# Optimization experiments

Measured on AMD Instinct MI355X. Metric: run time of the kernel, lower is better.

The kernel has to match this reference:

```python
import jax, jax.numpy as jnp
import numpy as np

B, S, D_MODEL, N_HEAD = 8, 512, 1024, 16
HEAD_DIM = D_MODEL // N_HEAD


def _pos_embed(seq_len, dim):
    # RelativeSinusoidalPositionalEmbedding(dim, padding_idx=0, init_size=1200)
    num = 1201  # init_size + 1
    half = dim // 2
    freq = np.exp(np.arange(half, dtype=np.float32) * (-np.log(10000.0) / (half - 1)))
    pos = np.arange(-((num + 1) // 2), num // 2, dtype=np.float32)  # tf.range(-num//2, num//2), python floor div
    emb = pos[:, None] * freq[None, :]
    table = np.concatenate([np.sin(emb), np.cos(emb)], axis=1).astype(np.float32)  # [num, dim]
    table[0] = 0.0  # padding_idx = 0
    origin_shift = num // 2 + 1  # 601
    idx = np.arange(-seq_len, seq_len) + origin_shift
    return jnp.asarray(table[idx])  # [2*seq_len, dim]


def setup_inputs() -> dict:
    key = jax.random.key(0)
    k1, k2, k3, k4 = jax.random.split(key, 4)
    return {
        "x": jax.random.normal(k1, (B, S, D_MODEL), dtype=jnp.float32),
        "mask": jnp.ones((B, S), dtype=jnp.int32),
        "Wqv": jax.random.normal(k2, (D_MODEL, 2 * D_MODEL), dtype=jnp.float32) * 0.02,
        "r_r_bias": jax.random.normal(k3, (N_HEAD, HEAD_DIM), dtype=jnp.float32) * 0.02,
        "r_w_bias": jax.random.normal(k4, (N_HEAD, HEAD_DIM), dtype=jnp.float32) * 0.02,
    }


def _shift(BD):
    # [b, h, s, 2s] -> [b, h, s, s] via pad-reshape trick
    b, h, s, _ = BD.shape
    zp = jnp.zeros((b, h, s, 1), BD.dtype)
    BD = jnp.concatenate([BD, zp], axis=-1).reshape(b, h, 2 * s + 1, s)
    BD = BD[:, :, :-1].reshape(b, h, s, 2 * s)
    return BD[:, :, :, s:]


def reference(x, mask, Wqv, r_r_bias, r_w_bias):
    pos = _pos_embed(S, HEAD_DIM)  # [2S, head_dim], stop-gradient constant
    qv = x @ Wqv  # [B, S, 2*D]
    q, v = jnp.split(qv, 2, axis=-1)

    def heads(t):
        return t.reshape(B, S, N_HEAD, HEAD_DIM).transpose(0, 2, 1, 3)  # bhsd

    q, k, v = heads(q), heads(x), heads(v)
    rw_q = q + r_r_bias[None, :, None, :]
    AC = jnp.einsum('bhqd,bhkd->bhqk', rw_q, k)
    D_ = jnp.einsum('hd,ld->hl', r_w_bias, pos)[None, :, None, :]  # [1, h, 1, 2S]
    B_ = jnp.einsum('bhqd,ld->bhql', q, pos)  # [b, h, S, 2S]
    BD = _shift(B_ + D_)
    attn = AC + BD  # scale=False -> divide by 1
    m = mask.astype(jnp.float32)[:, None, None, :]
    attn = attn * m - (1.0 - m) * 1e8
    attn = jax.nn.softmax(attn, axis=-1)  # dropout is identity at inference
    out = jnp.einsum('bhqk,bhkd->bhqd', attn, v)
    return out.transpose(0, 2, 1, 3).reshape(B, S, D_MODEL)
```

## Files before the change

kernel.cpp:

```cpp
#include <hip/hip_runtime.h>


using h4 = __attribute__((ext_vector_type(4))) _Float16;
using h8 = __attribute__((ext_vector_type(8))) _Float16;
using f32x4 = __attribute__((ext_vector_type(4))) float;

#define MFMA16(a, b, c) __builtin_amdgcn_mfma_f32_16x16x32_f16((a), (b), (c), 0, 0, 0)

#define GLOAD_LDS16(gp, lp)                                                        \
  __builtin_amdgcn_global_load_lds(                                                \
      (const __attribute__((address_space(1))) unsigned int*)(gp),                 \
      (__attribute__((address_space(3))) unsigned int*)(lp), 16, 0, 0)

__global__ __launch_bounds__(256) void k_cast_x(const float* __restrict__ x,
                                                _Float16* __restrict__ xh) {
  size_t idx = (size_t)blockIdx.x * 256 + threadIdx.x;
  const float* src = x + idx * 8;
  _Float16 tmp[8];
#pragma unroll
  for (int j = 0; j < 8; ++j) tmp[j] = (_Float16)src[j];
  *(h8*)(xh + idx * 8) = *(const h8*)tmp;
}

__global__ __launch_bounds__(256) void k_posP(_Float16* __restrict__ posP) {
  int idx = blockIdx.x * 256 + threadIdx.x;
  int t = idx >> 6, j = idx & 63;
  int jj = j & 31;
  float f = expf((float)jj * (-9.210340371976184f / 31.0f));
  float ang = (float)t * f;
  posP[idx] = (_Float16)((j < 32) ? sinf(ang) : cosf(ang));
}

__global__ __launch_bounds__(256) void k_trans_w(const float* __restrict__ Wqv,
                                                 _Float16* __restrict__ wT) {
  __shared__ _Float16 t[64][72];
  int bk = blockIdx.x & 15, bn = blockIdx.x >> 4;
  int k0 = bk * 64, n0 = bn * 64;
  int r = threadIdx.x >> 2, c = (threadIdx.x & 3) * 16;
  const float* src = Wqv + (size_t)(k0 + r) * 2048 + n0 + c;
#pragma unroll
  for (int j = 0; j < 16; ++j) t[r][c + j] = (_Float16)src[j];
  __syncthreads();
  _Float16 tmp[16];
#pragma unroll
  for (int j = 0; j < 16; ++j) tmp[j] = t[c + j][r];
  _Float16* dst = wT + (size_t)(n0 + r) * 1024 + k0 + c;
  *(h8*)dst = *(const h8*)tmp;
  *(h8*)(dst + 8) = *(const h8*)(tmp + 8);
}

__global__ __launch_bounds__(256) void k_gemm(const _Float16* __restrict__ xh,
                                              const _Float16* __restrict__ wT,
                                              const float* __restrict__ rr,
                                              const float* __restrict__ rw,
                                              _Float16* __restrict__ qrr,
                                              _Float16* __restrict__ qrwp,
                                              _Float16* __restrict__ vT) {
  __shared__ _Float16 At[128 * 32];
  __shared__ _Float16 Bt[128 * 32];

  int bid = blockIdx.x;
  int bm = bid & 31, bn = bid >> 5;
  int tid = threadIdx.x;
  int w = tid >> 6, lane = tid & 63;
  int lr = lane & 15, lg = lane >> 4;

  const _Float16* gA = xh + (size_t)(bm * 128 + 32 * w + (lane >> 2)) * 1024 + (lane & 3) * 8;
  const _Float16* gB = wT + (size_t)(bn * 128 + 32 * w + (lane >> 2)) * 1024 + (lane & 3) * 8;
  _Float16* lA0 = &At[(32 * w) * 32];
  _Float16* lA1 = &At[(32 * w + 16) * 32];
  _Float16* lB0 = &Bt[(32 * w) * 32];
  _Float16* lB1 = &Bt[(32 * w + 16) * 32];

  int wm = w >> 1, wn = w & 1;
  const _Float16* la = &At[(wm * 64 + lr) * 32 + lg * 8];
  const _Float16* lb = &Bt[(wn * 64 + lr) * 32 + lg * 8];

  f32x4 acc[4][4] = {};

  for (int k0 = 0; k0 < 1024; k0 += 32) {
    GLOAD_LDS16(gA + k0, lA0);
    GLOAD_LDS16(gA + 16 * 1024 + k0, lA1);
    GLOAD_LDS16(gB + k0, lB0);
    GLOAD_LDS16(gB + 16 * 1024 + k0, lB1);
    __syncthreads();
    h8 af[4], bf[4];
#pragma unroll
    for (int mi = 0; mi < 4; ++mi) af[mi] = *(const h8*)(la + mi * 512);
#pragma unroll
    for (int ni = 0; ni < 4; ++ni) bf[ni] = *(const h8*)(lb + ni * 512);
#pragma unroll
    for (int mi = 0; mi < 4; ++mi)
#pragma unroll
      for (int ni = 0; ni < 4; ++ni)
        acc[mi][ni] = MFMA16(af[mi], bf[ni], acc[mi][ni]);
    __syncthreads();
  }

  int hg = bn * 2 + wn;
  int mb = bm * 128 + wm * 64;
  if (hg < 16) {
    int h = hg;
    float rrv[4], rwv[4];
#pragma unroll
    for (int ni = 0; ni < 4; ++ni) {
      rrv[ni] = rr[h * 64 + ni * 16 + lr];
      rwv[ni] = rw[h * 64 + ni * 16 + lr];
    }
    float f0 = expf((float)lr * (-9.210340371976184f / 31.0f));
    float f1 = expf((float)(16 + lr) * (-9.210340371976184f / 31.0f));
#pragma unroll
    for (int mi = 0; mi < 4; ++mi)
#pragma unroll
      for (int r = 0; r < 4; ++r) {
        int m = mb + mi * 16 + lg * 4 + r;
        int b = m >> 9, s = m & 511;
        size_t base = ((size_t)(b * 16 + h) * 512 + s) * 64;
#pragma unroll
        for (int ni = 0; ni < 4; ++ni)
          qrr[base + ni * 16 + lr] = (_Float16)(acc[mi][ni][r] + rrv[ni]);
        {
          float qs = acc[mi][0][r] + rwv[0], qc = acc[mi][2][r] + rwv[2];
          float sn, cs;
          sincosf((float)s * f0, &sn, &cs);
          qrwp[base + lr] = (_Float16)(qs * cs + qc * sn);
          qrwp[base + lr + 32] = (_Float16)(qc * cs - qs * sn);
        }
        {
          float qs = acc[mi][1][r] + rwv[1], qc = acc[mi][3][r] + rwv[3];
          float sn, cs;
          sincosf((float)s * f1, &sn, &cs);
          qrwp[base + 16 + lr] = (_Float16)(qs * cs + qc * sn);
          qrwp[base + 16 + lr + 32] = (_Float16)(qc * cs - qs * sn);
        }
      }
  } else {
    int h = hg - 16;
#pragma unroll
    for (int mi = 0; mi < 4; ++mi) {
      int m = mb + mi * 16 + lg * 4;
      int b = m >> 9, s0 = m & 511;
      size_t vtbase = (size_t)(b * 16 + h) * 64 * 512;
#pragma unroll
      for (int ni = 0; ni < 4; ++ni) {
        int d = ni * 16 + lr;
        _Float16 t4[4];
#pragma unroll
        for (int r = 0; r < 4; ++r) t4[r] = (_Float16)acc[mi][ni][r];
        *(h4*)(vT + vtbase + (size_t)d * 512 + s0) = *(const h4*)t4;
      }
    }
  }
}

__global__ __launch_bounds__(256, 2) void k_attn(const _Float16* __restrict__ xh,
                                                 const _Float16* __restrict__ qrr,
                                                 const _Float16* __restrict__ qrwp,
                                                 const _Float16* __restrict__ vT,
                                                 const _Float16* __restrict__ posPg,
                                                 const int* __restrict__ mask,
                                                 float* __restrict__ out) {
  __shared__ _Float16 Kp[128 * 128];
  __shared__ _Float16 Vt[64 * 128];
  __shared__ _Float16 Pl[4][16 * 136];
  __shared__ float Ms[512];

  int bid = blockIdx.x;
  int qb = bid >> 7, h = bid & 15, b = (bid >> 4) & 7;
  int q0 = qb * 64;
  int tid = threadIdx.x;
  int w = tid >> 6, lane = tid & 63;
  int lr = lane & 15, lg = lane >> 4;

  const size_t bh = (size_t)(b * 16 + h);
  const _Float16* qrr_p = qrr + (bh * 512 + q0 + 16 * w + lr) * 64 + lg * 8;
  const _Float16* qrw_p = qrwp + (bh * 512 + q0 + 16 * w + lr) * 64 + lg * 8;
  const _Float16* kb = xh + (size_t)b * 512 * 1024 + h * 64;
  const _Float16* vTp = vT + bh * 64 * 512;
  const int* mrow = mask + b * 512;

  Ms[tid] = (float)mrow[tid];
  Ms[tid + 256] = (float)mrow[tid + 256];

  h8 ar0 = *(const h8*)(qrr_p);
  h8 ar1 = *(const h8*)(qrr_p + 32);
  h8 aw0 = *(const h8*)(qrw_p);
  h8 aw1 = *(const h8*)(qrw_p + 32);

  float m_run[4], l_run[4];
  f32x4 O[4];
#pragma unroll
  for (int r = 0; r < 4; ++r) { m_run[r] = -1e30f; l_run[r] = 0.f; }
#pragma unroll
  for (int df = 0; df < 4; ++df) O[df] = (f32x4){0.f, 0.f, 0.f, 0.f};

  _Float16* pw = &Pl[w][0];

  for (int t0 = 0; t0 < 512; t0 += 128) {
#pragma unroll
    for (int it = 0; it < 8; ++it) {
      int a = w * 512 + it * 64 + lane;
      int trow = a >> 4, c16 = a & 15;
      int c16s = c16 ^ (trow & 15);
      const _Float16* g = (c16s < 8)
          ? kb + (size_t)(t0 + trow) * 1024 + c16s * 8
          : posPg + (size_t)(t0 + trow) * 64 + (c16s - 8) * 8;
      GLOAD_LDS16(g, &Kp[(size_t)(w * 512 + it * 64) * 8]);
    }
#pragma unroll
    for (int it = 0; it < 4; ++it) {
      int a = w * 256 + it * 64 + lane;
      int drow = a >> 4, c16 = a & 15;
      int c16s = c16 ^ (drow & 15);
      const _Float16* g = vTp + (size_t)drow * 512 + t0 + c16s * 8;
      GLOAD_LDS16(g, &Vt[(size_t)(w * 256 + it * 64) * 8]);
    }
    __syncthreads();

    float s[8][4];
#pragma unroll
    for (int tf = 0; tf < 8; ++tf) {
      int row = tf * 16 + lr;
      const _Float16* bp = &Kp[row * 128];
      h8 b0 = *(const h8*)(bp + ((0 + lg) ^ lr) * 8);
      h8 b1 = *(const h8*)(bp + ((4 + lg) ^ lr) * 8);
      h8 b2 = *(const h8*)(bp + ((8 + lg) ^ lr) * 8);
      h8 b3 = *(const h8*)(bp + ((12 + lg) ^ lr) * 8);
      f32x4 c = {0.f, 0.f, 0.f, 0.f};
      c = MFMA16(ar0, b0, c);
      c = MFMA16(ar1, b1, c);
      c = MFMA16(aw0, b2, c);
      c = MFMA16(aw1, b3, c);
      float mm = Ms[t0 + tf * 16 + lr];
#pragma unroll
      for (int r = 0; r < 4; ++r) s[tf][r] = c[r] * mm - (1.f - mm) * 1e8f;
    }

#pragma unroll
    for (int r = 0; r < 4; ++r) {
      float rm = s[0][r];
#pragma unroll
      for (int tf = 1; tf < 8; ++tf) rm = fmaxf(rm, s[tf][r]);
#pragma unroll
      for (int d = 1; d < 16; d <<= 1) rm = fmaxf(rm, __shfl_xor(rm, d));
      float mn = fmaxf(m_run[r], rm);
      float sc = __expf(m_run[r] - mn);
      m_run[r] = mn;
      float rs = 0.f;
#pragma unroll
      for (int tf = 0; tf < 8; ++tf) {
        float p = __expf(s[tf][r] - mn);
        _Float16 p16 = (_Float16)p;
        pw[(lg * 4 + r) * 136 + tf * 16 + lr] = p16;
        rs += (float)p16;
      }
#pragma unroll
      for (int d = 1; d < 16; d <<= 1) rs += __shfl_xor(rs, d);
      l_run[r] = l_run[r] * sc + rs;
#pragma unroll
      for (int df = 0; df < 4; ++df) O[df][r] *= sc;
    }

    h8 pa[4];
#pragma unroll
    for (int ks = 0; ks < 4; ++ks)
      pa[ks] = *(const h8*)(pw + lr * 136 + ks * 32 + lg * 8);
#pragma unroll
    for (int df = 0; df < 4; ++df) {
      int row = df * 16 + lr;
      const _Float16* vbp = &Vt[row * 128];
#pragma unroll
      for (int ks = 0; ks < 4; ++ks) {
        h8 vb = *(const h8*)(vbp + ((ks * 4 + lg) ^ lr) * 8);
        O[df] = MFMA16(pa[ks], vb, O[df]);
      }
    }
    __syncthreads();
  }

#pragma unroll
  for (int df = 0; df < 4; ++df)
#pragma unroll
    for (int r = 0; r < 4; ++r) {
      int ii = 16 * w + lg * 4 + r;
      out[((size_t)b * 512 + q0 + ii) * 1024 + h * 64 + df * 16 + lr] = O[df][r] / l_run[r];
    }
}

extern "C" void kernel_launch(void* const* d_in, const int* in_sizes, int n_in,
                              void* d_out, int out_size, void* d_ws, size_t ws_size,
                              hipStream_t stream) {
  const float* x = (const float*)d_in[0];
  const int* mask = (const int*)d_in[1];
  const float* Wqv = (const float*)d_in[2];
  const float* rr = (const float*)d_in[3];
  const float* rw = (const float*)d_in[4];
  float* out = (float*)d_out;
  char* ws = (char*)d_ws;
  const size_t MB = 1024 * 1024;
  _Float16* xh = (_Float16*)(ws);
  _Float16* wT = (_Float16*)(ws + 8 * MB);
  _Float16* posP = (_Float16*)(ws + 12 * MB);
  _Float16* qrr = (_Float16*)(ws + 13 * MB);
  _Float16* qrwp = (_Float16*)(ws + 21 * MB);
  _Float16* vT = (_Float16*)(ws + 29 * MB);

  k_cast_x<<<2048, 256, 0, stream>>>(x, xh);
  k_posP<<<128, 256, 0, stream>>>(posP);
  k_trans_w<<<512, 256, 0, stream>>>(Wqv, wT);
  k_gemm<<<512, 256, 0, stream>>>(xh, wT, rr, rw, qrr, qrwp, vT);
  k_attn<<<1024, 256, 0, stream>>>(xh, qrr, qrwp, vT, posP, mask, out);
}
```

Measured before the change: 80.07 us.

## Double-buffer GEMM and attention LDS tiles and merge prep kernels into one

The three preprocessing kernels (x cast, positional table, W transpose) are merged into a single launch dispatched by block index. This removes two kernel launches and the gaps between them. The GEMM main loop now double-buffers its A/B LDS tiles, prefetching the next K slice while MFMAs run on the current one. The attention kernel moves to 64-key tiles with double-buffered K/pos and V staging, smaller P scratch and an extra barrier, so global loads overlap compute. The price is more LDS per GEMM block and more loop iterations and barriers in attention.

Measured after the change: 84.69 us. 5.8% more time.

```diff
diff --git a/kernel.cpp b/kernel.cpp
--- a/kernel.cpp
+++ b/kernel.cpp
@@ -12,41 +12,44 @@
       (const __attribute__((address_space(1))) unsigned int*)(gp),                 \
       (__attribute__((address_space(3))) unsigned int*)(lp), 16, 0, 0)
 
-__global__ __launch_bounds__(256) void k_cast_x(const float* __restrict__ x,
-                                                _Float16* __restrict__ xh) {
-  size_t idx = (size_t)blockIdx.x * 256 + threadIdx.x;
-  const float* src = x + idx * 8;
-  _Float16 tmp[8];
-#pragma unroll
-  for (int j = 0; j < 8; ++j) tmp[j] = (_Float16)src[j];
-  *(h8*)(xh + idx * 8) = *(const h8*)tmp;
-}
-
-__global__ __launch_bounds__(256) void k_posP(_Float16* __restrict__ posP) {
-  int idx = blockIdx.x * 256 + threadIdx.x;
-  int t = idx >> 6, j = idx & 63;
-  int jj = j & 31;
-  float f = expf((float)jj * (-9.210340371976184f / 31.0f));
-  float ang = (float)t * f;
-  posP[idx] = (_Float16)((j < 32) ? sinf(ang) : cosf(ang));
-}
-
-__global__ __launch_bounds__(256) void k_trans_w(const float* __restrict__ Wqv,
-                                                 _Float16* __restrict__ wT) {
+__global__ __launch_bounds__(256) void k_prep(const float* __restrict__ x,
+                                              const float* __restrict__ Wqv,
+                                              _Float16* __restrict__ xh,
+                                              _Float16* __restrict__ wT,
+                                              _Float16* __restrict__ posP) {
   __shared__ _Float16 t[64][72];
-  int bk = blockIdx.x & 15, bn = blockIdx.x >> 4;
-  int k0 = bk * 64, n0 = bn * 64;
-  int r = threadIdx.x >> 2, c = (threadIdx.x & 3) * 16;
-  const float* src = Wqv + (size_t)(k0 + r) * 2048 + n0 + c;
-#pragma unroll
-  for (int j = 0; j < 16; ++j) t[r][c + j] = (_Float16)src[j];
-  __syncthreads();
-  _Float16 tmp[16];
-#pragma unroll
-  for (int j = 0; j < 16; ++j) tmp[j] = t[c + j][r];
-  _Float16* dst = wT + (size_t)(n0 + r) * 1024 + k0 + c;
-  *(h8*)dst = *(const h8*)tmp;
-  *(h8*)(dst + 8) = *(const h8*)(tmp + 8);
+  int bid = blockIdx.x;
+  int tid = threadIdx.x;
+  if (bid < 2048) {
+    size_t idx = (size_t)bid * 256 + tid;
+    const float* src = x + idx * 8;
+    _Float16 tmp[8];
+#pragma unroll
+    for (int j = 0; j < 8; ++j) tmp[j] = (_Float16)src[j];
+    *(h8*)(xh + idx * 8) = *(const h8*)tmp;
+  } else if (bid < 2176) {
+    int idx = (bid - 2048) * 256 + tid;
+    int tt = idx >> 6, j = idx & 63;
+    int jj = j & 31;
+    float f = expf((float)jj * (-9.210340371976184f / 31.0f));
+    float ang = (float)tt * f;
+    posP[idx] = (_Float16)((j < 32) ? sinf(ang) : cosf(ang));
+  } else {
+    int b2 = bid - 2176;
+    int bk = b2 & 15, bn = b2 >> 4;
+    int k0 = bk * 64, n0 = bn * 64;
+    int r = tid >> 2, c = (tid & 3) * 16;
+    const float* src = Wqv + (size_t)(k0 + r) * 2048 + n0 + c;
+#pragma unroll
+    for (int j = 0; j < 16; ++j) t[r][c + j] = (_Float16)src[j];
+    __syncthreads();
+    _Float16 tmp[16];
+#pragma unroll
+    for (int j = 0; j < 16; ++j) tmp[j] = t[c + j][r];
+    _Float16* dst = wT + (size_t)(n0 + r) * 1024 + k0 + c;
+    *(h8*)dst = *(const h8*)tmp;
+    *(h8*)(dst + 8) = *(const h8*)(tmp + 8);
+  }
 }
 
 __global__ __launch_bounds__(256) void k_gemm(const _Float16* __restrict__ xh,
@@ -56,8 +59,8 @@
                                               _Float16* __restrict__ qrr,
                                               _Float16* __restrict__ qrwp,
                                               _Float16* __restrict__ vT) {
-  __shared__ _Float16 At[128 * 32];
-  __shared__ _Float16 Bt[128 * 32];
+  __shared__ _Float16 At[2][128 * 32];
+  __shared__ _Float16 Bt[2][128 * 32];
 
   int bid = blockIdx.x;
   int bm = bid & 31, bn = bid >> 5;
@@ -67,23 +70,24 @@
 
   const _Float16* gA = xh + (size_t)(bm * 128 + 32 * w + (lane >> 2)) * 1024 + (lane & 3) * 8;
   const _Float16* gB = wT + (size_t)(bn * 128 + 32 * w + (lane >> 2)) * 1024 + (lane & 3) * 8;
-  _Float16* lA0 = &At[(32 * w) * 32];
-  _Float16* lA1 = &At[(32 * w + 16) * 32];
-  _Float16* lB0 = &Bt[(32 * w) * 32];
-  _Float16* lB1 = &Bt[(32 * w + 16) * 32];
+
+  auto stage = [&](int bufi, int k0) {
+    GLOAD_LDS16(gA + k0, &At[bufi][(32 * w) * 32]);
+    GLOAD_LDS16(gA + 16 * 1024 + k0, &At[bufi][(32 * w + 16) * 32]);
+    GLOAD_LDS16(gB + k0, &Bt[bufi][(32 * w) * 32]);
+    GLOAD_LDS16(gB + 16 * 1024 + k0, &Bt[bufi][(32 * w + 16) * 32]);
+  };
 
   int wm = w >> 1, wn = w & 1;
-  const _Float16* la = &At[(wm * 64 + lr) * 32 + lg * 8];
-  const _Float16* lb = &Bt[(wn * 64 + lr) * 32 + lg * 8];
-
   f32x4 acc[4][4] = {};
 
-  for (int k0 = 0; k0 < 1024; k0 += 32) {
-    GLOAD_LDS16(gA + k0, lA0);
-    GLOAD_LDS16(gA + 16 * 1024 + k0, lA1);
-    GLOAD_LDS16(gB + k0, lB0);
-    GLOAD_LDS16(gB + 16 * 1024 + k0, lB1);
-    __syncthreads();
+  stage(0, 0);
+  __syncthreads();
+  int buf = 0;
+  for (int i = 0; i < 32; ++i) {
+    if (i < 31) stage(buf ^ 1, (i + 1) * 32);
+    const _Float16* la = &At[buf][(wm * 64 + lr) * 32 + lg * 8];
+    const _Float16* lb = &Bt[buf][(wn * 64 + lr) * 32 + lg * 8];
     h8 af[4], bf[4];
 #pragma unroll
     for (int mi = 0; mi < 4; ++mi) af[mi] = *(const h8*)(la + mi * 512);
@@ -95,6 +99,7 @@
       for (int ni = 0; ni < 4; ++ni)
         acc[mi][ni] = MFMA16(af[mi], bf[ni], acc[mi][ni]);
     __syncthreads();
+    buf ^= 1;
   }
 
   int hg = bn * 2 + wn;
@@ -160,9 +165,9 @@
                                                  const _Float16* __restrict__ posPg,
                                                  const int* __restrict__ mask,
                                                  float* __restrict__ out) {
-  __shared__ _Float16 Kp[128 * 128];
-  __shared__ _Float16 Vt[64 * 128];
-  __shared__ _Float16 Pl[4][16 * 136];
+  __shared__ _Float16 Kp[2][64 * 128];
+  __shared__ _Float16 Vt[2][64 * 64];
+  __shared__ _Float16 Pl[4][16 * 72];
   __shared__ float Ms[512];
 
   int bid = blockIdx.x;
@@ -179,6 +184,27 @@
   const _Float16* vTp = vT + bh * 64 * 512;
   const int* mrow = mask + b * 512;
 
+  auto stage = [&](int bufi, int t0s) {
+#pragma unroll
+    for (int it = 0; it < 4; ++it) {
+      int a = w * 256 + it * 64 + lane;
+      int trow = a >> 4, c16 = a & 15;
+      int c16s = c16 ^ (trow & 15);
+      const _Float16* g = (c16s < 8)
+          ? kb + (size_t)(t0s + trow) * 1024 + c16s * 8
+          : posPg + (size_t)(t0s + trow) * 64 + (c16s - 8) * 8;
+      GLOAD_LDS16(g, &Kp[bufi][(w * 256 + it * 64) * 8]);
+    }
+#pragma unroll
+    for (int it = 0; it < 2; ++it) {
+      int a = w * 128 + it * 64 + lane;
+      int drow = a >> 3, c8 = a & 7;
+      int c8s = c8 ^ (drow & 7);
+      const _Float16* g = vTp + (size_t)drow * 512 + t0s + c8s * 8;
+      GLOAD_LDS16(g, &Vt[bufi][(w * 128 + it * 64) * 8]);
+    }
+  };
+
   Ms[tid] = (float)mrow[tid];
   Ms[tid + 256] = (float)mrow[tid + 256];
 
@@ -196,32 +222,18 @@
 
   _Float16* pw = &Pl[w][0];
 
-  for (int t0 = 0; t0 < 512; t0 += 128) {
-#pragma unroll
-    for (int it = 0; it < 8; ++it) {
-      int a = w * 512 + it * 64 + lane;
-      int trow = a >> 4, c16 = a & 15;
-      int c16s = c16 ^ (trow & 15);
-      const _Float16* g = (c16s < 8)
-          ? kb + (size_t)(t0 + trow) * 1024 + c16s * 8
-          : posPg + (size_t)(t0 + trow) * 64 + (c16s - 8) * 8;
-      GLOAD_LDS16(g, &Kp[(size_t)(w * 512 + it * 64) * 8]);
-    }
-#pragma unroll
-    for (int it = 0; it < 4; ++it) {
-      int a = w * 256 + it * 64 + lane;
-      int drow = a >> 4, c16 = a & 15;
-      int c16s = c16 ^ (drow & 15);
-      const _Float16* g = vTp + (size_t)drow * 512 + t0 + c16s * 8;
-      GLOAD_LDS16(g, &Vt[(size_t)(w * 256 + it * 64) * 8]);
-    }
-    __syncthreads();
-
-    float s[8][4];
-#pragma unroll
-    for (int tf = 0; tf < 8; ++tf) {
+  stage(0, 0);
+  __syncthreads();
+  int buf = 0;
+  for (int i = 0; i < 8; ++i) {
+    int t0 = i * 64;
+    if (i < 7) stage(buf ^ 1, t0 + 64);
+
+    float s[4][4];
+#pragma unroll
+    for (int tf = 0; tf < 4; ++tf) {
       int row = tf * 16 + lr;
-      const _Float16* bp = &Kp[row * 128];
+      const _Float16* bp = &Kp[buf][row * 128];
       h8 b0 = *(const h8*)(bp + ((0 + lg) ^ lr) * 8);
       h8 b1 = *(const h8*)(bp + ((4 + lg) ^ lr) * 8);
       h8 b2 = *(const h8*)(bp + ((8 + lg) ^ lr) * 8);
@@ -238,9 +250,7 @@
 
 #pragma unroll
     for (int r = 0; r < 4; ++r) {
-      float rm = s[0][r];
-#pragma unroll
-      for (int tf = 1; tf < 8; ++tf) rm = fmaxf(rm, s[tf][r]);
+      float rm = fmaxf(fmaxf(s[0][r], s[1][r]), fmaxf(s[2][r], s[3][r]));
 #pragma unroll
       for (int d = 1; d < 16; d <<= 1) rm = fmaxf(rm, __shfl_xor(rm, d));
       float mn = fmaxf(m_run[r], rm);
@@ -248,10 +258,10 @@
       m_run[r] = mn;
       float rs = 0.f;
 #pragma unroll
-      for (int tf = 0; tf < 8; ++tf) {
+      for (int tf = 0; tf < 4; ++tf) {
         float p = __expf(s[tf][r] - mn);
         _Float16 p16 = (_Float16)p;
-        pw[(lg * 4 + r) * 136 + tf * 16 + lr] = p16;
+        pw[(lg * 4 + r) * 72 + tf * 16 + lr] = p16;
         rs += (float)p16;
       }
 #pragma unroll
@@ -261,21 +271,22 @@
       for (int df = 0; df < 4; ++df) O[df][r] *= sc;
     }
 
-    h8 pa[4];
-#pragma unroll
-    for (int ks = 0; ks < 4; ++ks)
-      pa[ks] = *(const h8*)(pw + lr * 136 + ks * 32 + lg * 8);
+    asm volatile("s_waitcnt lgkmcnt(0)" ::: "memory");
+    __builtin_amdgcn_s_barrier();
+
+    h8 pa0 = *(const h8*)(pw + lr * 72 + lg * 8);
+    h8 pa1 = *(const h8*)(pw + lr * 72 + 32 + lg * 8);
 #pragma unroll
     for (int df = 0; df < 4; ++df) {
       int row = df * 16 + lr;
-      const _Float16* vbp = &Vt[row * 128];
-#pragma unroll
-      for (int ks = 0; ks < 4; ++ks) {
-        h8 vb = *(const h8*)(vbp + ((ks * 4 + lg) ^ lr) * 8);
-        O[df] = MFMA16(pa[ks], vb, O[df]);
-      }
+      const _Float16* vbp = &Vt[buf][row * 64];
+      h8 vb0 = *(const h8*)(vbp + ((0 + lg) ^ (lr & 7)) * 8);
+      h8 vb1 = *(const h8*)(vbp + ((4 + lg) ^ (lr & 7)) * 8);
+      O[df] = MFMA16(pa0, vb0, O[df]);
+      O[df] = MFMA16(pa1, vb1, O[df]);
     }
     __syncthreads();
+    buf ^= 1;
   }
 
 #pragma unroll
@@ -305,9 +316,7 @@
   _Float16* qrwp = (_Float16*)(ws + 21 * MB);
   _Float16* vT = (_Float16*)(ws + 29 * MB);
 
-  k_cast_x<<<2048, 256, 0, stream>>>(x, xh);
-  k_posP<<<128, 256, 0, stream>>>(posP);
-  k_trans_w<<<512, 256, 0, stream>>>(Wqv, wT);
+  k_prep<<<2688, 256, 0, stream>>>(x, Wqv, xh, wT, posP);
   k_gemm<<<512, 256, 0, stream>>>(xh, wT, rr, rw, qrr, qrwp, vT);
   k_attn<<<1024, 256, 0, stream>>>(xh, qrr, qrwp, vT, posP, mask, out);
 }
```
